# Kernel tuning notes

Measured on AMD Instinct MI355X. Metric: run time of the kernel, lower is better.

Reference implementation:

```python
import jax, jax.numpy as jnp
import numpy as np
import math

B, C, H, W = 32, 128, 32, 32
NUM_HEADS = 4
GROUPS = 32
EPS = 1e-5


def setup_inputs() -> dict:
    key = jax.random.key(0)
    ks = jax.random.split(key, 6)
    x = jax.random.normal(ks[0], (B, C, H, W), jnp.float32)
    norm_w = 1.0 + 0.1 * jax.random.normal(ks[1], (C,), jnp.float32)
    norm_b = 0.1 * jax.random.normal(ks[2], (C,), jnp.float32)
    qkv_w = jax.random.normal(ks[3], (3 * C, C), jnp.float32) / math.sqrt(C)
    proj_w = jax.random.normal(ks[4], (C, C), jnp.float32) / math.sqrt(C)
    proj_b = 0.01 * jax.random.normal(ks[5], (C,), jnp.float32)
    return {"x": x, "norm_w": norm_w, "norm_b": norm_b, "qkv_w": qkv_w,
            "proj_w": proj_w, "proj_b": proj_b}


def _group_norm(x, w, b):
    b_, c, h, w_ = x.shape
    xg = x.reshape(b_, GROUPS, c // GROUPS, h, w_)
    mu = xg.mean(axis=(2, 3, 4), keepdims=True)
    var = xg.var(axis=(2, 3, 4), keepdims=True)
    xn = ((xg - mu) * jax.lax.rsqrt(var + EPS)).reshape(b_, c, h, w_)
    return xn * w[None, :, None, None] + b[None, :, None, None]


def reference(x, norm_w, norm_b, qkv_w, proj_w, proj_b):
    b, c, h, w = x.shape
    nh = NUM_HEADS
    dh = c // nh
    hw = h * w
    xn = _group_norm(x, norm_w, norm_b)
    # 1x1 conv (no bias): [B,3C,H,W] flattened to [B,3C,HW]
    qkv = jnp.einsum('oc,bchw->bohw', qkv_w, xn).reshape(b, nh, 3 * dh, hw)
    # torch reshape (B*nh, 3C/nh, HW) + chunk(3, dim=1): per-head interleave
    q, k, v = qkv[:, :, :dh], qkv[:, :, dh:2 * dh], qkv[:, :, 2 * dh:]
    scale = 1.0 / math.sqrt(dh)
    # scale applied to BOTH q and k, as in the source
    attn = jnp.einsum('bhct,bhcs->bhts', q * scale, k * scale)  # [B,nh,HW,HW]
    attn = jax.nn.softmax(attn, axis=-1)
    hout = jnp.einsum('bhts,bhcs->bhct', attn, v).reshape(b, c, h, w)
    hout = jnp.einsum('oc,bchw->bohw', proj_w, hout) + proj_b[None, :, None, None]
    return hout + x
```

## Files before the change

### kernel.cpp

```cpp
#include <hip/hip_runtime.h>
#include <math.h>

#define BB 32
#define CC 128
#define HW 1024
#define NG 32
#define TPG 4096
#define QSZ ((size_t)BB * 4 * HW * 32)

typedef __attribute__((ext_vector_type(8))) short fragAB;
typedef __attribute__((ext_vector_type(4))) float fragC;
typedef __attribute__((ext_vector_type(8))) ushort ushort8v;

__device__ __forceinline__ ushort f2bf(float f) {
  union { float f; uint u; } v; v.f = f;
  uint r = v.u + 0x7FFFu + ((v.u >> 16) & 1u);
  return (ushort)(r >> 16);
}
__device__ __forceinline__ uint pack2(float lo, float hi) {
  return __builtin_amdgcn_perm(__float_as_uint(hi), __float_as_uint(lo), 0x07060302u);
}
__device__ __forceinline__ float bflo(uint u) { return __uint_as_float(u << 16); }
__device__ __forceinline__ float bfhi(uint u) { return __uint_as_float(u & 0xffff0000u); }
__device__ __forceinline__ int vswz(int row, int g) {
  return row * 128 + 16 * (g ^ (row & 7));
}

__global__ __launch_bounds__(256) void gn_stats(const float* __restrict__ x,
    float2* __restrict__ stats, const float* __restrict__ qkvw,
    const float* __restrict__ projw, ushort* __restrict__ wq16,
    ushort* __restrict__ wp16) {
  if (blockIdx.x >= 1024) {
    int idx = (blockIdx.x - 1024) * 256 + threadIdx.x;
    if (idx < 49152) wq16[idx] = f2bf(qkvw[idx]);
    else             wp16[idx - 49152] = f2bf(projw[idx - 49152]);
    return;
  }
  int blk = blockIdx.x;
  int b = blk >> 5, g = blk & 31;
  const float4* xp4 = (const float4*)(x + ((size_t)(b * CC + g * 4)) * HW);
  float s = 0.f, s2 = 0.f;
  #pragma unroll
  for (int i = 0; i < 4; ++i) {
    float4 v = xp4[threadIdx.x + i * 256];
    s  += v.x + v.y + v.z + v.w;
    s2 += v.x * v.x + v.y * v.y + v.z * v.z + v.w * v.w;
  }
  #pragma unroll
  for (int off = 32; off; off >>= 1) {
    s  += __shfl_down(s, off, 64);
    s2 += __shfl_down(s2, off, 64);
  }
  __shared__ float ls[4], ls2[4];
  int lane = threadIdx.x & 63, wid = threadIdx.x >> 6;
  if (lane == 0) { ls[wid] = s; ls2[wid] = s2; }
  __syncthreads();
  if (threadIdx.x == 0) {
    float a  = ls[0] + ls[1] + ls[2] + ls[3];
    float a2 = ls2[0] + ls2[1] + ls2[2] + ls2[3];
    float mu = a * (1.f / TPG);
    float var = a2 * (1.f / TPG) - mu * mu;
    stats[blk] = make_float2(mu, rsqrtf(var + 1e-5f));
  }
}

template<int PROJ>
__global__ __launch_bounds__(256) void mgemm(
    const ushort* __restrict__ W16, const ushort* __restrict__ X16,
    const float* __restrict__ xf, const float2* __restrict__ stats,
    const float* __restrict__ gw, const float* __restrict__ gb,
    ushort* __restrict__ Qb, float* __restrict__ out,
    const float* __restrict__ bias, const float* __restrict__ resid) {
  __shared__ ushort Xs[64 * 128];
  int b = blockIdx.z, o0 = blockIdx.y * 64, t0 = blockIdx.x * 64;
  int tid = threadIdx.x;
  int lane = tid & 63, w = tid >> 6, lc = lane & 15, lg = lane >> 4;
  int wo = w >> 1, wt = w & 1;

  fragAB af[2][4];
  #pragma unroll
  for (int i = 0; i < 2; ++i)
    #pragma unroll
    for (int kc = 0; kc < 4; ++kc)
      af[i][kc] = *(const fragAB*)&W16[(size_t)(o0 + wo * 32 + i * 16 + lc) * 128 + kc * 32 + lg * 8];

  if constexpr (PROJ == 0) {
    int tq = tid & 15, co = tid >> 4;
    const float* xb = xf + (size_t)b * CC * HW + t0 + tq * 4;
    float wsc[8], bsc[8];
    {
      float2 s0 = stats[b * 32 + co * 2];
      float2 s1 = stats[b * 32 + co * 2 + 1];
      #pragma unroll
      for (int cc = 0; cc < 8; ++cc) {
        float rst = (cc < 4) ? s0.y : s1.y;
        float mu  = (cc < 4) ? s0.x : s1.x;
        float g = gw[co * 8 + cc];
        wsc[cc] = g * rst;
        bsc[cc] = gb[co * 8 + cc] - mu * wsc[cc];
      }
    }
    union { float4 v; float f[4]; } vv[8];
    #pragma unroll
    for (int cc = 0; cc < 8; ++cc)
      vv[cc].v = *(const float4*)&xb[(size_t)(co * 8 + cc) * HW];
    #pragma unroll
    for (int tt = 0; tt < 4; ++tt) {
      int row = tq * 4 + tt;
      ushort8v r;
      #pragma unroll
      for (int cc = 0; cc < 8; ++cc)
        r[cc] = f2bf(vv[cc].f[tt] * wsc[cc] + bsc[cc]);
      int byt = (row * 256 + co * 16) ^ ((row & 7) << 4);
      *(ushort8v*)((char*)Xs + byt) = r;
    }
  } else {
    const char* src = (const char*)(X16 + ((size_t)b * HW + t0) * CC);
    char* dst = (char*)Xs;
    #pragma unroll
    for (int it = 0; it < 4; ++it) {
      int flat = tid * 16 + it * 4096;
      uint4 v = *(const uint4*)(src + flat);
      *(uint4*)(dst + (flat ^ (((flat >> 8) & 7) << 4))) = v;
    }
  }
  __syncthreads();

  fragC acc[2][2];
  #pragma unroll
  for (int i = 0; i < 2; ++i)
    #pragma unroll
    for (int j = 0; j < 2; ++j)
      acc[i][j] = (fragC){0.f, 0.f, 0.f, 0.f};

  #pragma unroll
  for (int kc = 0; kc < 4; ++kc) {
    fragAB bf[2];
    #pragma unroll
    for (int j = 0; j < 2; ++j) {
      int row = wt * 32 + j * 16 + lc;
      int byt = (row * 256 + kc * 64 + lg * 16) ^ ((row & 7) << 4);
      bf[j] = *(const fragAB*)((const char*)Xs + byt);
    }
    #pragma unroll
    for (int i = 0; i < 2; ++i)
      #pragma unroll
      for (int j = 0; j < 2; ++j)
        acc[i][j] = __builtin_amdgcn_mfma_f32_16x16x32_bf16(af[i][kc], bf[j], acc[i][j], 0, 0, 0);
  }

  if constexpr (PROJ == 0) {
    #pragma unroll
    for (int i = 0; i < 2; ++i) {
      int ob = o0 + wo * 32 + i * 16;
      int blk = ob >> 5;
      int hh = blk / 3, kind = blk % 3;
      size_t bh = (size_t)b * 4 + hh;
      float sc = (kind == 0) ? (0.03125f * 1.44269504f) : 1.f;
      #pragma unroll
      for (int j = 0; j < 2; ++j) {
        if (kind < 2) {
          ushort* dst = (kind == 0) ? Qb : (Qb + QSZ);
          int s16 = (t0 >> 4) + wt * 2 + j;
          int eo = s16 * 512 + (((ob & 16) >> 3) + (lg >> 1)) * 128 + lc * 8 + (lg & 1) * 4;
          ushort4 rv;
          rv.x = f2bf(acc[i][j][0] * sc); rv.y = f2bf(acc[i][j][1] * sc);
          rv.z = f2bf(acc[i][j][2] * sc); rv.w = f2bf(acc[i][j][3] * sc);
          *(ushort4*)&dst[bh * 32768 + eo] = rv;
        } else {
          ushort* Vb = Qb + 2 * QSZ;
          int eo = (t0 >> 6) * 2048 + ((ob & 16) >> 4) * 1024
                 + (wt * 4 + j * 2 + (lc >> 3)) * 128 + (lc & 7);
          #pragma unroll
          for (int r = 0; r < 4; ++r)
            Vb[bh * 32768 + eo + (lg * 4 + r) * 8] = f2bf(acc[i][j][r]);
        }
      }
    }
  } else {
    #pragma unroll
    for (int i = 0; i < 2; ++i)
      #pragma unroll
      for (int j = 0; j < 2; ++j) {
        int t = t0 + wt * 32 + j * 16 + lc;
        #pragma unroll
        for (int r = 0; r < 4; ++r) {
          int o = o0 + wo * 32 + i * 16 + lg * 4 + r;
          size_t idx = ((size_t)b * CC + o) * HW + t;
          out[idx] = acc[i][j][r] + bias[o] + resid[idx];
        }
      }
  }
}

__global__ __launch_bounds__(256) void attn7(
    const ushort* __restrict__ Qb, const ushort* __restrict__ Kb,
    const ushort* __restrict__ Vb, ushort* __restrict__ ao16) {
  __shared__ char arena[16384];

  int tid = threadIdx.x;
  int w = tid >> 6, lane = tid & 63, lc = lane & 15, lg = lane >> 4;
  int lb = blockIdx.x;
  int gp = (lb & 7) * 256 + (lb >> 3);
  int bh = gp >> 4, qp = gp & 15;
  int h = bh & 3, b = bh >> 2;
  int qt = qp * 2 + (w >> 1);
  int sh = w & 1;
  int t0 = qt * 32;

  const ushort* Qg = Qb + (size_t)bh * 32768 + (size_t)qt * 1024 + lane * 8;
  const ushort* Kg = Kb + (size_t)bh * 32768 + lane * 8;
  const ushort* Vg = Vb + (size_t)bh * 32768 + lane * 8;

  fragAB q0 = *(const fragAB*)&Qg[0];
  fragAB q1 = *(const fragAB*)&Qg[512];

  fragC a00 = {0.f,0.f,0.f,0.f}, a01 = {0.f,0.f,0.f,0.f};
  fragC a10 = {0.f,0.f,0.f,0.f}, a11 = {0.f,0.f,0.f,0.f};
  float l0 = 0.f, l1 = 0.f;
  char* wreg = arena + w * 4096;

  for (int i = sh * 8; i < sh * 8 + 8; ++i) {
    const ushort* Kt = Kg + i * 2048;
    const ushort* Vt = Vg + i * 2048;
    fragAB kf[4], vf[4];
    #pragma unroll
    for (int j = 0; j < 4; ++j) kf[j] = *(const fragAB*)&Kt[j * 512];
    #pragma unroll
    for (int u = 0; u < 4; ++u) vf[u] = *(const fragAB*)&Vt[u * 512];

    #pragma unroll
    for (int ts = 0; ts < 2; ++ts) {
      fragAB qf = ts ? q1 : q0;
      char* PsB = wreg + ts * 2048;
      fragC S[4];
      #pragma unroll
      for (int j = 0; j < 4; ++j) {
        fragC z = {0.f,0.f,0.f,0.f};
        S[j] = __builtin_amdgcn_mfma_f32_16x16x32_bf16(kf[j], qf, z, 0, 0, 0);
      }
      float rs = 0.f;
      #pragma unroll
      for (int j = 0; j < 4; ++j) {
        float p0 = __builtin_amdgcn_exp2f(S[j][0]), p1 = __builtin_amdgcn_exp2f(S[j][1]);
        float p2 = __builtin_amdgcn_exp2f(S[j][2]), p3 = __builtin_amdgcn_exp2f(S[j][3]);
        rs += (p0 + p1) + (p2 + p3);
        uint2 wv2;
        wv2.x = pack2(p0, p1);
        wv2.y = pack2(p2, p3);
        int g = j * 2 + (lg >> 1);
        *(uint2*)(PsB + lc * 128 + 16 * (g ^ (lc & 7)) + (lg & 1) * 8) = wv2;
      }
      if (ts) l1 += rs; else l0 += rs;
      fragC* aA = ts ? &a01 : &a00;
      fragC* aB = ts ? &a11 : &a10;
      fragAB bp0 = *(const fragAB*)(PsB + vswz(lc, lg));
      fragAB bp1 = *(const fragAB*)(PsB + vswz(lc, 4 + lg));
      *aA = __builtin_amdgcn_mfma_f32_16x16x32_bf16(vf[0], bp0, *aA, 0, 0, 0);
      *aA = __builtin_amdgcn_mfma_f32_16x16x32_bf16(vf[1], bp1, *aA, 0, 0, 0);
      *aB = __builtin_amdgcn_mfma_f32_16x16x32_bf16(vf[2], bp0, *aB, 0, 0, 0);
      *aB = __builtin_amdgcn_mfma_f32_16x16x32_bf16(vf[3], bp1, *aB, 0, 0, 0);
    }
  }

  if (sh == 1) {
    char* slot = wreg + lane * 40;
    uint2 u;
    u.x = pack2(a00[0], a00[1]); u.y = pack2(a00[2], a00[3]);
    *(uint2*)(slot) = u;
    u.x = pack2(a10[0], a10[1]); u.y = pack2(a10[2], a10[3]);
    *(uint2*)(slot + 8) = u;
    u.x = pack2(a01[0], a01[1]); u.y = pack2(a01[2], a01[3]);
    *(uint2*)(slot + 16) = u;
    u.x = pack2(a11[0], a11[1]); u.y = pack2(a11[2], a11[3]);
    *(uint2*)(slot + 24) = u;
    *(float2*)(slot + 32) = make_float2(l0, l1);
  }
  __syncthreads();
  if (sh == 1) return;

  {
    const char* slot = arena + (w + 1) * 4096 + lane * 40;
    uint2 u0 = *(const uint2*)(slot);
    uint2 u1 = *(const uint2*)(slot + 8);
    uint2 u2 = *(const uint2*)(slot + 16);
    uint2 u3 = *(const uint2*)(slot + 24);
    float2 lv = *(const float2*)(slot + 32);
    a00[0] += bflo(u0.x); a00[1] += bfhi(u0.x); a00[2] += bflo(u0.y); a00[3] += bfhi(u0.y);
    a10[0] += bflo(u1.x); a10[1] += bfhi(u1.x); a10[2] += bflo(u1.y); a10[3] += bfhi(u1.y);
    a01[0] += bflo(u2.x); a01[1] += bfhi(u2.x); a01[2] += bflo(u2.y); a01[3] += bfhi(u2.y);
    a11[0] += bflo(u3.x); a11[1] += bfhi(u3.x); a11[2] += bflo(u3.y); a11[3] += bfhi(u3.y);
    l0 += lv.x; l1 += lv.y;
  }

  l0 += __shfl_xor(l0, 16); l0 += __shfl_xor(l0, 32);
  l1 += __shfl_xor(l1, 16); l1 += __shfl_xor(l1, 32);
  float il0 = 1.f / l0, il1 = 1.f / l1;

  ushort* Ol = (ushort*)wreg;
  uint2 u;
  u.x = pack2(a00[0] * il0, a00[1] * il0); u.y = pack2(a00[2] * il0, a00[3] * il0);
  *(uint2*)&Ol[lc * 40 + lg * 4] = u;
  u.x = pack2(a10[0] * il0, a10[1] * il0); u.y = pack2(a10[2] * il0, a10[3] * il0);
  *(uint2*)&Ol[lc * 40 + 16 + lg * 4] = u;
  u.x = pack2(a01[0] * il1, a01[1] * il1); u.y = pack2(a01[2] * il1, a01[3] * il1);
  *(uint2*)&Ol[(lc + 16) * 40 + lg * 4] = u;
  u.x = pack2(a11[0] * il1, a11[1] * il1); u.y = pack2(a11[2] * il1, a11[3] * il1);
  *(uint2*)&Ol[(lc + 16) * 40 + 16 + lg * 4] = u;

  int row = lane >> 1, half = lane & 1;
  uint4 v0 = *(uint4*)&Ol[row * 40 + half * 16];
  uint4 v1 = *(uint4*)&Ol[row * 40 + half * 16 + 8];
  ushort* dst = &ao16[((size_t)b * HW + t0 + row) * CC + h * 32 + half * 16];
  *(uint4*)dst = v0;
  *(uint4*)(dst + 8) = v1;
}

extern "C" void kernel_launch(void* const* d_in, const int* in_sizes, int n_in,
                              void* d_out, int out_size, void* d_ws, size_t ws_size,
                              hipStream_t stream) {
  (void)in_sizes; (void)n_in; (void)out_size; (void)ws_size;
  const float* x     = (const float*)d_in[0];
  const float* gw    = (const float*)d_in[1];
  const float* gb    = (const float*)d_in[2];
  const float* qkvw  = (const float*)d_in[3];
  const float* projw = (const float*)d_in[4];
  const float* projb = (const float*)d_in[5];
  float* out = (float*)d_out;

  char* wsb = (char*)d_ws;
  ushort* ao16 = (ushort*)wsb;
  ushort* Qb   = (ushort*)(wsb + ((size_t)8 << 20));
  ushort* Kb   = Qb + QSZ;
  ushort* Vb   = Qb + 2 * QSZ;
  ushort* wq16 = (ushort*)(wsb + ((size_t)32 << 20));
  ushort* wp16 = (ushort*)(wsb + ((size_t)32 << 20) + (128 << 10));
  float2* stats = (float2*)(wsb + ((size_t)32 << 20) + (256 << 10));

  gn_stats<<<dim3(BB * NG + 256), 256, 0, stream>>>(x, stats, qkvw, projw, wq16, wp16);
  mgemm<0><<<dim3(16, 6, BB), 256, 0, stream>>>(wq16, nullptr, x, stats, gw, gb,
                                                Qb, nullptr, nullptr, nullptr);
  attn7<<<dim3(2048), 256, 0, stream>>>(Qb, Kb, Vb, ao16);
  mgemm<1><<<dim3(16, 2, BB), 256, 0, stream>>>(wp16, ao16, nullptr, nullptr, nullptr, nullptr,
                                                nullptr, out, projb, x);
}
```

Before: 69.80 us.

## Fuse output projection into attention and compute all QKV rows per block

The QKV GEMM now runs one block per 64-token tile and loops over all six 64-row output chunks, double-buffering weight fragments. This normalizes x once per tile instead of six times. The attention kernel now uses 512 threads covering all four heads of a 32-query tile, stages the normalized head outputs in shared memory, and applies the output projection, bias and residual directly. This removes the ao16 round trip and one kernel launch, at the cost of fewer, larger blocks and more register and LDS pressure.

```diff
diff --git a/kernel.cpp b/kernel.cpp
--- a/kernel.cpp
+++ b/kernel.cpp
@@ -64,27 +64,17 @@
   }
 }
 
-template<int PROJ>
-__global__ __launch_bounds__(256) void mgemm(
-    const ushort* __restrict__ W16, const ushort* __restrict__ X16,
-    const float* __restrict__ xf, const float2* __restrict__ stats,
-    const float* __restrict__ gw, const float* __restrict__ gb,
-    ushort* __restrict__ Qb, float* __restrict__ out,
-    const float* __restrict__ bias, const float* __restrict__ resid) {
+__global__ __launch_bounds__(256) void mgemm_qkv(
+    const ushort* __restrict__ W16, const float* __restrict__ xf,
+    const float2* __restrict__ stats, const float* __restrict__ gw,
+    const float* __restrict__ gb, ushort* __restrict__ Qb) {
   __shared__ ushort Xs[64 * 128];
-  int b = blockIdx.z, o0 = blockIdx.y * 64, t0 = blockIdx.x * 64;
+  int b = blockIdx.z, t0 = blockIdx.x * 64;
   int tid = threadIdx.x;
   int lane = tid & 63, w = tid >> 6, lc = lane & 15, lg = lane >> 4;
   int wo = w >> 1, wt = w & 1;
 
-  fragAB af[2][4];
-  #pragma unroll
-  for (int i = 0; i < 2; ++i)
-    #pragma unroll
-    for (int kc = 0; kc < 4; ++kc)
-      af[i][kc] = *(const fragAB*)&W16[(size_t)(o0 + wo * 32 + i * 16 + lc) * 128 + kc * 32 + lg * 8];
-
-  if constexpr (PROJ == 0) {
+  {
     int tq = tid & 15, co = tid >> 4;
     const float* xb = xf + (size_t)b * CC * HW + t0 + tq * 4;
     float wsc[8], bsc[8];
@@ -114,42 +104,39 @@
       int byt = (row * 256 + co * 16) ^ ((row & 7) << 4);
       *(ushort8v*)((char*)Xs + byt) = r;
     }
-  } else {
-    const char* src = (const char*)(X16 + ((size_t)b * HW + t0) * CC);
-    char* dst = (char*)Xs;
-    #pragma unroll
-    for (int it = 0; it < 4; ++it) {
-      int flat = tid * 16 + it * 4096;
-      uint4 v = *(const uint4*)(src + flat);
-      *(uint4*)(dst + (flat ^ (((flat >> 8) & 7) << 4))) = v;
-    }
   }
   __syncthreads();
 
-  fragC acc[2][2];
-  #pragma unroll
-  for (int i = 0; i < 2; ++i)
-    #pragma unroll
-    for (int j = 0; j < 2; ++j)
-      acc[i][j] = (fragC){0.f, 0.f, 0.f, 0.f};
-
-  #pragma unroll
-  for (int kc = 0; kc < 4; ++kc) {
-    fragAB bf[2];
-    #pragma unroll
-    for (int j = 0; j < 2; ++j) {
-      int row = wt * 32 + j * 16 + lc;
-      int byt = (row * 256 + kc * 64 + lg * 16) ^ ((row & 7) << 4);
-      bf[j] = *(const fragAB*)((const char*)Xs + byt);
-    }
+  auto load_af = [&](fragAB af[2][4], int o0) {
     #pragma unroll
     for (int i = 0; i < 2; ++i)
       #pragma unroll
+      for (int kc = 0; kc < 4; ++kc)
+        af[i][kc] = *(const fragAB*)&W16[(size_t)(o0 + wo * 32 + i * 16 + lc) * 128 + kc * 32 + lg * 8];
+  };
+  auto kloop = [&](fragAB af[2][4], fragC acc[2][2]) {
+    #pragma unroll
+    for (int i = 0; i < 2; ++i)
+      #pragma unroll
       for (int j = 0; j < 2; ++j)
-        acc[i][j] = __builtin_amdgcn_mfma_f32_16x16x32_bf16(af[i][kc], bf[j], acc[i][j], 0, 0, 0);
-  }
-
-  if constexpr (PROJ == 0) {
+        acc[i][j] = (fragC){0.f, 0.f, 0.f, 0.f};
+    #pragma unroll
+    for (int kc = 0; kc < 4; ++kc) {
+      fragAB bf[2];
+      #pragma unroll
+      for (int j = 0; j < 2; ++j) {
+        int row = wt * 32 + j * 16 + lc;
+        int byt = (row * 256 + kc * 64 + lg * 16) ^ ((row & 7) << 4);
+        bf[j] = *(const fragAB*)((const char*)Xs + byt);
+      }
+      #pragma unroll
+      for (int i = 0; i < 2; ++i)
+        #pragma unroll
+        for (int j = 0; j < 2; ++j)
+          acc[i][j] = __builtin_amdgcn_mfma_f32_16x16x32_bf16(af[i][kc], bf[j], acc[i][j], 0, 0, 0);
+    }
+  };
+  auto epi = [&](fragC acc[2][2], int o0) {
     #pragma unroll
     for (int i = 0; i < 2; ++i) {
       int ob = o0 + wo * 32 + i * 16;
@@ -177,35 +164,34 @@
         }
       }
     }
-  } else {
-    #pragma unroll
-    for (int i = 0; i < 2; ++i)
-      #pragma unroll
-      for (int j = 0; j < 2; ++j) {
-        int t = t0 + wt * 32 + j * 16 + lc;
-        #pragma unroll
-        for (int r = 0; r < 4; ++r) {
-          int o = o0 + wo * 32 + i * 16 + lg * 4 + r;
-          size_t idx = ((size_t)b * CC + o) * HW + t;
-          out[idx] = acc[i][j][r] + bias[o] + resid[idx];
-        }
-      }
-  }
-}
-
-__global__ __launch_bounds__(256) void attn7(
+  };
+
+  fragAB afA[2][4], afB[2][4];
+  fragC acc[2][2];
+  load_af(afA, 0);
+  load_af(afB, 64);
+  kloop(afA, acc); epi(acc, 0);   load_af(afA, 128);
+  kloop(afB, acc); epi(acc, 64);  load_af(afB, 192);
+  kloop(afA, acc); epi(acc, 128); load_af(afA, 256);
+  kloop(afB, acc); epi(acc, 192); load_af(afB, 320);
+  kloop(afA, acc); epi(acc, 256);
+  kloop(afB, acc); epi(acc, 320);
+}
+
+__global__ __launch_bounds__(512) void attn8(
     const ushort* __restrict__ Qb, const ushort* __restrict__ Kb,
-    const ushort* __restrict__ Vb, ushort* __restrict__ ao16) {
-  __shared__ char arena[16384];
+    const ushort* __restrict__ Vb, const ushort* __restrict__ wp16,
+    const float* __restrict__ bias, const float* __restrict__ resid,
+    float* __restrict__ out) {
+  __shared__ char arena[27136];
 
   int tid = threadIdx.x;
   int w = tid >> 6, lane = tid & 63, lc = lane & 15, lg = lane >> 4;
   int lb = blockIdx.x;
-  int gp = (lb & 7) * 256 + (lb >> 3);
-  int bh = gp >> 4, qp = gp & 15;
-  int h = bh & 3, b = bh >> 2;
-  int qt = qp * 2 + (w >> 1);
-  int sh = w & 1;
+  int gp = (lb & 7) * 128 + (lb >> 3);
+  int b = gp >> 5, qt = gp & 31;
+  int h = w >> 1, sh = w & 1;
+  int bh = b * 4 + h;
   int t0 = qt * 32;
 
   const ushort* Qg = Qb + (size_t)bh * 32768 + (size_t)qt * 1024 + lane * 8;
@@ -218,7 +204,7 @@
   fragC a00 = {0.f,0.f,0.f,0.f}, a01 = {0.f,0.f,0.f,0.f};
   fragC a10 = {0.f,0.f,0.f,0.f}, a11 = {0.f,0.f,0.f,0.f};
   float l0 = 0.f, l1 = 0.f;
-  char* wreg = arena + w * 4096;
+  char* PsB = arena + w * 2048;
 
   for (int i = sh * 8; i < sh * 8 + 8; ++i) {
     const ushort* Kt = Kg + i * 2048;
@@ -232,7 +218,6 @@
     #pragma unroll
     for (int ts = 0; ts < 2; ++ts) {
       fragAB qf = ts ? q1 : q0;
-      char* PsB = wreg + ts * 2048;
       fragC S[4];
       #pragma unroll
       for (int j = 0; j < 4; ++j) {
@@ -263,8 +248,9 @@
     }
   }
 
+  float2* lpart = (float2*)(arena + 16384);
   if (sh == 1) {
-    char* slot = wreg + lane * 40;
+    char* slot = PsB + lane * 32;
     uint2 u;
     u.x = pack2(a00[0], a00[1]); u.y = pack2(a00[2], a00[3]);
     *(uint2*)(slot) = u;
@@ -274,46 +260,61 @@
     *(uint2*)(slot + 16) = u;
     u.x = pack2(a11[0], a11[1]); u.y = pack2(a11[2], a11[3]);
     *(uint2*)(slot + 24) = u;
-    *(float2*)(slot + 32) = make_float2(l0, l1);
+    lpart[h * 64 + lane] = make_float2(l0, l1);
   }
   __syncthreads();
-  if (sh == 1) return;
-
-  {
-    const char* slot = arena + (w + 1) * 4096 + lane * 40;
+
+  ushort* Olds = (ushort*)(arena + 18432);
+  if (sh == 0) {
+    const char* slot = arena + (w + 1) * 2048 + lane * 32;
     uint2 u0 = *(const uint2*)(slot);
     uint2 u1 = *(const uint2*)(slot + 8);
     uint2 u2 = *(const uint2*)(slot + 16);
     uint2 u3 = *(const uint2*)(slot + 24);
-    float2 lv = *(const float2*)(slot + 32);
+    float2 lv = lpart[h * 64 + lane];
     a00[0] += bflo(u0.x); a00[1] += bfhi(u0.x); a00[2] += bflo(u0.y); a00[3] += bfhi(u0.y);
     a10[0] += bflo(u1.x); a10[1] += bfhi(u1.x); a10[2] += bflo(u1.y); a10[3] += bfhi(u1.y);
     a01[0] += bflo(u2.x); a01[1] += bfhi(u2.x); a01[2] += bflo(u2.y); a01[3] += bfhi(u2.y);
     a11[0] += bflo(u3.x); a11[1] += bfhi(u3.x); a11[2] += bflo(u3.y); a11[3] += bfhi(u3.y);
     l0 += lv.x; l1 += lv.y;
-  }
-
-  l0 += __shfl_xor(l0, 16); l0 += __shfl_xor(l0, 32);
-  l1 += __shfl_xor(l1, 16); l1 += __shfl_xor(l1, 32);
-  float il0 = 1.f / l0, il1 = 1.f / l1;
-
-  ushort* Ol = (ushort*)wreg;
-  uint2 u;
-  u.x = pack2(a00[0] * il0, a00[1] * il0); u.y = pack2(a00[2] * il0, a00[3] * il0);
-  *(uint2*)&Ol[lc * 40 + lg * 4] = u;
-  u.x = pack2(a10[0] * il0, a10[1] * il0); u.y = pack2(a10[2] * il0, a10[3] * il0);
-  *(uint2*)&Ol[lc * 40 + 16 + lg * 4] = u;
-  u.x = pack2(a01[0] * il1, a01[1] * il1); u.y = pack2(a01[2] * il1, a01[3] * il1);
-  *(uint2*)&Ol[(lc + 16) * 40 + lg * 4] = u;
-  u.x = pack2(a11[0] * il1, a11[1] * il1); u.y = pack2(a11[2] * il1, a11[3] * il1);
-  *(uint2*)&Ol[(lc + 16) * 40 + 16 + lg * 4] = u;
-
-  int row = lane >> 1, half = lane & 1;
-  uint4 v0 = *(uint4*)&Ol[row * 40 + half * 16];
-  uint4 v1 = *(uint4*)&Ol[row * 40 + half * 16 + 8];
-  ushort* dst = &ao16[((size_t)b * HW + t0 + row) * CC + h * 32 + half * 16];
-  *(uint4*)dst = v0;
-  *(uint4*)(dst + 8) = v1;
+
+    l0 += __shfl_xor(l0, 16); l0 += __shfl_xor(l0, 32);
+    l1 += __shfl_xor(l1, 16); l1 += __shfl_xor(l1, 32);
+    float il0 = 1.f / l0, il1 = 1.f / l1;
+
+    int cb = h * 32;
+    uint2 u;
+    u.x = pack2(a00[0] * il0, a00[1] * il0); u.y = pack2(a00[2] * il0, a00[3] * il0);
+    *(uint2*)&Olds[lc * 136 + cb + lg * 4] = u;
+    u.x = pack2(a10[0] * il0, a10[1] * il0); u.y = pack2(a10[2] * il0, a10[3] * il0);
+    *(uint2*)&Olds[lc * 136 + cb + 16 + lg * 4] = u;
+    u.x = pack2(a01[0] * il1, a01[1] * il1); u.y = pack2(a01[2] * il1, a01[3] * il1);
+    *(uint2*)&Olds[(lc + 16) * 136 + cb + lg * 4] = u;
+    u.x = pack2(a11[0] * il1, a11[1] * il1); u.y = pack2(a11[2] * il1, a11[3] * il1);
+    *(uint2*)&Olds[(lc + 16) * 136 + cb + 16 + lg * 4] = u;
+  }
+  __syncthreads();
+
+  fragC pacc[2] = {{0.f,0.f,0.f,0.f}, {0.f,0.f,0.f,0.f}};
+  #pragma unroll
+  for (int kc = 0; kc < 4; ++kc) {
+    fragAB af = *(const fragAB*)&wp16[(size_t)(16 * w + lc) * 128 + kc * 32 + lg * 8];
+    #pragma unroll
+    for (int j = 0; j < 2; ++j) {
+      fragAB bf = *(const fragAB*)&Olds[(j * 16 + lc) * 136 + kc * 32 + lg * 8];
+      pacc[j] = __builtin_amdgcn_mfma_f32_16x16x32_bf16(af, bf, pacc[j], 0, 0, 0);
+    }
+  }
+  #pragma unroll
+  for (int j = 0; j < 2; ++j) {
+    int t = t0 + j * 16 + lc;
+    #pragma unroll
+    for (int r = 0; r < 4; ++r) {
+      int o = 16 * w + lg * 4 + r;
+      size_t idx = ((size_t)b * CC + o) * HW + t;
+      out[idx] = pacc[j][r] + bias[o] + resid[idx];
+    }
+  }
 }
 
 extern "C" void kernel_launch(void* const* d_in, const int* in_sizes, int n_in,
@@ -329,7 +330,6 @@
   float* out = (float*)d_out;
 
   char* wsb = (char*)d_ws;
-  ushort* ao16 = (ushort*)wsb;
   ushort* Qb   = (ushort*)(wsb + ((size_t)8 << 20));
   ushort* Kb   = Qb + QSZ;
   ushort* Vb   = Qb + 2 * QSZ;
@@ -338,9 +338,6 @@
   float2* stats = (float2*)(wsb + ((size_t)32 << 20) + (256 << 10));
 
   gn_stats<<<dim3(BB * NG + 256), 256, 0, stream>>>(x, stats, qkvw, projw, wq16, wp16);
-  mgemm<0><<<dim3(16, 6, BB), 256, 0, stream>>>(wq16, nullptr, x, stats, gw, gb,
-                                                Qb, nullptr, nullptr, nullptr);
-  attn7<<<dim3(2048), 256, 0, stream>>>(Qb, Kb, Vb, ao16);
-  mgemm<1><<<dim3(16, 2, BB), 256, 0, stream>>>(wp16, ao16, nullptr, nullptr, nullptr, nullptr,
-                                                nullptr, out, projb, x);
-}
+  mgemm_qkv<<<dim3(16, 1, BB), 256, 0, stream>>>(wq16, x, stats, gw, gb, Qb);
+  attn8<<<dim3(1024), 512, 0, stream>>>(Qb, Kb, Vb, wp16, projb, x, out);
+}
```

New measurement: 60.16 us. 1.16x faster.
